# Kernel tuning notes

Measured on AMD Instinct MI355X. Metric: run time of the kernel, lower is better.

Reference implementation:

```python
import jax, jax.numpy as jnp
import numpy as np

N, E = 50000, 800000
F_IN, F_EMB1, F_EMB2, F_HID, F_OUT = 128, 512, 128, 1024, 64


def _linear_params(k, fan_in, fan_out):
    s = 1.0 / np.sqrt(fan_in)
    kw, kb = jax.random.split(k)
    W = jax.random.uniform(kw, (fan_in, fan_out), jnp.float32, -s, s)
    b = jax.random.uniform(kb, (fan_out,), jnp.float32, -s, s)
    return W, b


def setup_inputs() -> dict:
    key = jax.random.key(0)
    ks = jax.random.split(key, 8)
    x = jax.random.normal(ks[0], (N, F_IN), jnp.float32)
    src = jax.random.randint(ks[1], (E,), 0, N)
    dst = jax.random.randint(ks[2], (E,), 0, N)
    edge_index = jnp.stack([src, dst])  # [2, E]
    edge_weight = jax.random.uniform(ks[3], (E,), jnp.float32)  # positive weights
    W1, b1 = _linear_params(ks[4], F_IN, F_EMB1)
    W2, b2 = _linear_params(ks[5], F_EMB1, F_EMB2)
    W3, b3 = _linear_params(ks[6], F_EMB2, F_HID)
    W4, b4 = _linear_params(ks[7], F_HID, F_OUT)
    return dict(x=x, edge_index=edge_index, edge_weight=edge_weight,
                W1=W1, b1=b1, W2=W2, b2=b2, W3=W3, b3=b3, W4=W4, b4=b4)


def gcn_conv(x, src, dst, w, W, b):
    """PyG GCNConv: transform, then sym-normalized weighted aggregation with self-loops.
    out = D^{-1/2} (A_w + I) D^{-1/2} (x W) + b,  deg = scatter(w @ dst) + 1."""
    n = x.shape[0]
    h = x @ W  # [N, F_out]
    deg = jax.ops.segment_sum(w, dst, num_segments=n) + 1.0  # +1 for self-loop weight
    dinv = jax.lax.rsqrt(deg)
    norm = dinv[src] * w * dinv[dst]  # [E]
    agg = jax.ops.segment_sum(norm[:, None] * h[src], dst, num_segments=n)
    agg = agg + h / deg[:, None]  # self-loop: dinv[i]*1*dinv[i] * h[i]
    return agg + b


def reference(x, edge_index, edge_weight, W1, b1, W2, b2, W3, b3, W4, b4):
    src, dst = edge_index[0], edge_index[1]
    h = jax.nn.relu(gcn_conv(x, src, dst, edge_weight, W1, b1))
    # graph_normalization=False -> identity; dropout is identity in eval mode
    h = jax.nn.relu(gcn_conv(h, src, dst, edge_weight, W2, b2))
    h = jax.nn.relu(h @ W3 + b3)
    out = jax.nn.relu(h @ W4 + b4)
    return out
```

## Files before the change

kernel.cpp:

```cpp
#include <hip/hip_runtime.h>


#define ELLW 64

typedef short bf16x8 __attribute__((ext_vector_type(8)));
typedef float f32x4 __attribute__((ext_vector_type(4)));

__device__ __forceinline__ unsigned short f2b(float f) {
    unsigned u = __builtin_bit_cast(unsigned, f);
    unsigned r = (u + 0x7FFFu + ((u >> 16) & 1u)) >> 16;
    return (unsigned short)r;
}
__device__ __forceinline__ float b2f(unsigned short u) {
    return __builtin_bit_cast(float, (unsigned)u << 16);
}

__global__ void k_setup(const float* __restrict__ x,
                        const float* __restrict__ W1, const float* __restrict__ W2,
                        const float* __restrict__ W3, const float* __restrict__ W4,
                        unsigned short* __restrict__ W1t, unsigned short* __restrict__ W2t,
                        unsigned short* __restrict__ W3t, unsigned short* __restrict__ W4t,
                        unsigned short* __restrict__ xb,
                        const int* __restrict__ src, const int* __restrict__ dst,
                        const float* __restrict__ ew,
                        unsigned long long* __restrict__ cnt64,
                        int2* __restrict__ s_edge, int Nn, int E) {
    int b = blockIdx.x;
    if (b < 3125) {
        int e = b * 256 + threadIdx.x;
        if (e < E) {
            int d = dst[e];
            float wv = ew[e];
            unsigned wfix = (unsigned)(wv * 8388608.0f);
            unsigned long long add = ((unsigned long long)1 << 32) | wfix;
            unsigned long long old = atomicAdd(&cnt64[d], add);
            int slot = (int)(old >> 32);
            if (slot < ELLW)
                s_edge[(size_t)d * ELLW + slot] =
                    make_int2(src[e], __builtin_bit_cast(int, wv));
        }
    } else if (b < 4405) {
        int i = (b - 3125) * 256 + threadIdx.x;
        if (i < 65536) {
            int k = i >> 9, n = i & 511;
            W1t[n * 128 + k] = f2b(W1[i]);
        } else if (i < 131072) {
            int j = i - 65536; int k = j >> 7, n = j & 127;
            W2t[n * 512 + k] = f2b(W2[j]);
        } else if (i < 262144) {
            int j = i - 131072; int k = j >> 10, n = j & 1023;
            W3t[n * 128 + k] = f2b(W3[j]);
        } else {
            int j = i - 262144; int k = j >> 6, n = j & 63;
            W4t[n * 1024 + k] = f2b(W4[j]);
        }
    } else {
        int i = (b - 4405) * 256 + threadIdx.x;
        if (i < Nn * 32) {
            float4 v = ((const float4*)x)[i];
            ushort4 o;
            o.x = f2b(v.x); o.y = f2b(v.y); o.z = f2b(v.z); o.w = f2b(v.w);
            ((ushort4*)xb)[i] = o;
        }
    }
}

__global__ __launch_bounds__(256) void k_degscale(
    const unsigned long long* __restrict__ cnt64, float* __restrict__ dinv,
    unsigned short* __restrict__ xb, int Nn) {
    int node = blockIdx.x * 4 + (threadIdx.x >> 6);
    if (node >= Nn) return;
    int lane = threadIdx.x & 63;
    unsigned long long cv = cnt64[node];
    float deg = 1.0f + (float)(unsigned)(cv & 0xFFFFFFFFull) * (1.0f / 8388608.0f);
    float di = rsqrtf(deg);
    if (lane == 0) dinv[node] = di;
    ushort2 v = ((ushort2*)(xb + (size_t)node * 128))[lane];
    ushort2 o;
    o.x = f2b(b2f(v.x) * di);
    o.y = f2b(b2f(v.y) * di);
    ((ushort2*)(xb + (size_t)node * 128))[lane] = o;
}

template <bool BIAS_RELU>
__global__ __launch_bounds__(256) void k_gather(
    const unsigned short* __restrict__ Xb, const int2* __restrict__ s_edge,
    const unsigned long long* __restrict__ cnt64, const float* __restrict__ dinv,
    const float* __restrict__ bias, unsigned short* __restrict__ outb, int Nn) {
    int node = blockIdx.x * 4 + (threadIdx.x >> 6);
    if (node >= Nn) return;
    int lane = threadIdx.x & 63;
    float di = dinv[node];
    ushort2 sv = ((const ushort2*)(Xb + (size_t)node * 128))[lane];
    float ax = b2f(sv.x), ay = b2f(sv.y);

    int c = min((int)(cnt64[node] >> 32), ELLW);
    size_t base = (size_t)node * ELLW;
    int sreg = 0;
    float nv = 0.0f;
    if (lane < c) {
        int2 rec = s_edge[base + lane];
        sreg = rec.x;
        nv = __builtin_bit_cast(float, rec.y);
    }

    int j = 0;
    for (; j + 8 <= c; j += 8) {
        int s0 = __shfl(sreg, j),     s1 = __shfl(sreg, j + 1);
        int s2 = __shfl(sreg, j + 2), s3 = __shfl(sreg, j + 3);
        int s4 = __shfl(sreg, j + 4), s5 = __shfl(sreg, j + 5);
        int s6 = __shfl(sreg, j + 6), s7 = __shfl(sreg, j + 7);
        float n0 = __shfl(nv, j),     n1 = __shfl(nv, j + 1);
        float n2 = __shfl(nv, j + 2), n3 = __shfl(nv, j + 3);
        float n4 = __shfl(nv, j + 4), n5 = __shfl(nv, j + 5);
        float n6 = __shfl(nv, j + 6), n7 = __shfl(nv, j + 7);
        ushort2 r0 = ((const ushort2*)(Xb + (size_t)s0 * 128))[lane];
        ushort2 r1 = ((const ushort2*)(Xb + (size_t)s1 * 128))[lane];
        ushort2 r2 = ((const ushort2*)(Xb + (size_t)s2 * 128))[lane];
        ushort2 r3 = ((const ushort2*)(Xb + (size_t)s3 * 128))[lane];
        ushort2 r4 = ((const ushort2*)(Xb + (size_t)s4 * 128))[lane];
        ushort2 r5 = ((const ushort2*)(Xb + (size_t)s5 * 128))[lane];
        ushort2 r6 = ((const ushort2*)(Xb + (size_t)s6 * 128))[lane];
        ushort2 r7 = ((const ushort2*)(Xb + (size_t)s7 * 128))[lane];
        ax += n0 * b2f(r0.x) + n1 * b2f(r1.x) + n2 * b2f(r2.x) + n3 * b2f(r3.x);
        ay += n0 * b2f(r0.y) + n1 * b2f(r1.y) + n2 * b2f(r2.y) + n3 * b2f(r3.y);
        ax += n4 * b2f(r4.x) + n5 * b2f(r5.x) + n6 * b2f(r6.x) + n7 * b2f(r7.x);
        ay += n4 * b2f(r4.y) + n5 * b2f(r5.y) + n6 * b2f(r6.y) + n7 * b2f(r7.y);
    }
    for (; j < c; ++j) {
        int sj = __shfl(sreg, j);
        float nj = __shfl(nv, j);
        ushort2 r = ((const ushort2*)(Xb + (size_t)sj * 128))[lane];
        ax += nj * b2f(r.x);
        ay += nj * b2f(r.y);
    }

    ax *= di; ay *= di;
    if (BIAS_RELU) {
        float2 bv = ((const float2*)bias)[lane];
        ax = fmaxf(ax + bv.x, 0.0f);
        ay = fmaxf(ay + bv.y, 0.0f);
    }
    ushort2 o; o.x = f2b(ax); o.y = f2b(ay);
    ((ushort2*)(outb + (size_t)node * 128))[lane] = o;
}

template <int H, int OUTW, bool HAS_BO, bool OUT_BF16, bool SCALE_OUT>
__global__ __launch_bounds__(256) void k_mlp(
    const unsigned short* __restrict__ A, const unsigned short* __restrict__ Wht,
    const unsigned short* __restrict__ Wot, const float* __restrict__ bh,
    const float* __restrict__ bo, const float* __restrict__ dinv,
    void* __restrict__ out, int M) {
    constexpr int HC = H / 64;
    constexpr int NJ = OUTW / 16;
    constexpr int OW4 = OUTW / 32;
    __shared__ __align__(16) unsigned short Whs[64 * 128];
    __shared__ __align__(16) unsigned short Ps[128 * 64];
    __shared__ __align__(16) unsigned short Wos[OUTW * 64];
    const int tid = threadIdx.x, wave = tid >> 6, lane = tid & 63;
    const int lm = lane & 15, quad = lane >> 4;
    const int bm0 = blockIdx.x * 128;

    bf16x8 af[2][4];
    #pragma unroll
    for (int i = 0; i < 2; ++i) {
        int gr = bm0 + wave * 32 + i * 16 + lm;
        #pragma unroll
        for (int kb = 0; kb < 4; ++kb) af[i][kb] = bf16x8{0, 0, 0, 0, 0, 0, 0, 0};
        if (gr < M) {
            #pragma unroll
            for (int kb = 0; kb < 4; ++kb)
                af[i][kb] = *(const bf16x8*)(A + (size_t)gr * 128 + kb * 32 + quad * 8);
        }
    }

    #pragma unroll
    for (int u = 0; u < 4; ++u) {
        int idx = tid + u * 256; int r = idx >> 4, g = idx & 15;
        *(int4*)&Whs[r * 128 + ((g ^ (r & 15)) * 8)] =
            *(const int4*)(Wht + (size_t)r * 128 + g * 8);
    }
    #pragma unroll
    for (int u = 0; u < OW4; ++u) {
        int idx = tid + u * 256; int r = idx >> 3, g = idx & 7;
        *(int4*)&Wos[r * 64 + ((g ^ (r & 7)) * 8)] =
            *(const int4*)(Wot + (size_t)r * H + g * 8);
    }
    __syncthreads();

    f32x4 oacc[2][NJ] = {};
    for (int c = 0; c < HC; ++c) {
        f32x4 hacc[2][4] = {};
        #pragma unroll
        for (int kb = 0; kb < 4; ++kb) {
            bf16x8 bfr[4];
            #pragma unroll
            for (int j = 0; j < 4; ++j) {
                int r = j * 16 + lm, g = kb * 4 + quad;
                bfr[j] = *(const bf16x8*)&Whs[r * 128 + ((g ^ (r & 15)) * 8)];
            }
            #pragma unroll
            for (int i = 0; i < 2; ++i)
                #pragma unroll
                for (int j = 0; j < 4; ++j)
                    hacc[i][j] = __builtin_amdgcn_mfma_f32_16x16x32_bf16(
                        af[i][kb], bfr[j], hacc[i][j], 0, 0, 0);
        }

        #pragma unroll
        for (int i = 0; i < 2; ++i) {
            #pragma unroll
            for (int j = 0; j < 4; ++j) {
                int col = j * 16 + lm;
                float bv = bh[c * 64 + col];
                #pragma unroll
                for (int r4 = 0; r4 < 4; ++r4) {
                    int row = wave * 32 + i * 16 + quad * 4 + r4;
                    float o = fmaxf(hacc[i][j][r4] + bv, 0.0f);
                    Ps[row * 64 + (((col >> 3) ^ (row & 7)) * 8) + (col & 7)] = f2b(o);
                }
            }
        }

        #pragma unroll
        for (int kb = 0; kb < 2; ++kb) {
            bf16x8 pf[2];
            #pragma unroll
            for (int i = 0; i < 2; ++i) {
                int r = wave * 32 + i * 16 + lm, g = kb * 4 + quad;
                pf[i] = *(const bf16x8*)&Ps[r * 64 + ((g ^ (r & 7)) * 8)];
            }
            #pragma unroll
            for (int j = 0; j < NJ; ++j) {
                int r = j * 16 + lm, g = kb * 4 + quad;
                bf16x8 wf = *(const bf16x8*)&Wos[r * 64 + ((g ^ (r & 7)) * 8)];
                #pragma unroll
                for (int i = 0; i < 2; ++i)
                    oacc[i][j] = __builtin_amdgcn_mfma_f32_16x16x32_bf16(
                        pf[i], wf, oacc[i][j], 0, 0, 0);
            }
        }

        if (c + 1 < HC) {
            __syncthreads();
            #pragma unroll
            for (int u = 0; u < 4; ++u) {
                int idx = tid + u * 256; int r = idx >> 4, g = idx & 15;
                *(int4*)&Whs[r * 128 + ((g ^ (r & 15)) * 8)] =
                    *(const int4*)(Wht + (size_t)((c + 1) * 64 + r) * 128 + g * 8);
            }
            #pragma unroll
            for (int u = 0; u < OW4; ++u) {
                int idx = tid + u * 256; int r = idx >> 3, g = idx & 7;
                *(int4*)&Wos[r * 64 + ((g ^ (r & 7)) * 8)] =
                    *(const int4*)(Wot + (size_t)r * H + (c + 1) * 64 + g * 8);
            }
            __syncthreads();
        }
    }

    #pragma unroll
    for (int i = 0; i < 2; ++i) {
        #pragma unroll
        for (int j = 0; j < NJ; ++j) {
            int col = j * 16 + lm;
            float bv = HAS_BO ? bo[col] : 0.0f;
            #pragma unroll
            for (int r4 = 0; r4 < 4; ++r4) {
                int m = bm0 + wave * 32 + i * 16 + quad * 4 + r4;
                if (m < M) {
                    float o = oacc[i][j][r4];
                    if (SCALE_OUT) o *= dinv[m];
                    if (HAS_BO) o = fmaxf(o + bv, 0.0f);
                    if (OUT_BF16)
                        ((unsigned short*)out)[(size_t)m * OUTW + col] = f2b(o);
                    else
                        ((float*)out)[(size_t)m * OUTW + col] = o;
                }
            }
        }
    }
}

static inline int cdiv(long a, long b) { return (int)((a + b - 1) / b); }

extern "C" void kernel_launch(void* const* d_in, const int* in_sizes, int n_in,
                              void* d_out, int out_size, void* d_ws, size_t ws_size,
                              hipStream_t stream) {
    const float* x  = (const float*)d_in[0];
    const int*   ei = (const int*)d_in[1];
    const float* ew = (const float*)d_in[2];
    const float* W1 = (const float*)d_in[3];
    const float* b1 = (const float*)d_in[4];
    const float* W2 = (const float*)d_in[5];
    const float* b2 = (const float*)d_in[6];
    const float* W3 = (const float*)d_in[7];
    const float* b3 = (const float*)d_in[8];
    const float* W4 = (const float*)d_in[9];
    const float* b4 = (const float*)d_in[10];
    const int Nn = in_sizes[0] / 128;
    const int E  = in_sizes[1] / 2;
    const int* src = ei;
    const int* dst = ei + E;

    char* ws = (char*)d_ws;
    size_t off_b = 0;
    auto alloc = [&](size_t bytes) -> void* {
        void* p = ws + off_b;
        off_b += (bytes + 255) & ~(size_t)255;
        return p;
    };
    float*              dinv   = (float*)alloc((size_t)Nn * 4);
    unsigned long long* cnt64  = (unsigned long long*)alloc((size_t)Nn * 8);
    int2*               s_edge = (int2*)alloc((size_t)Nn * ELLW * 8);
    unsigned short*     W1t    = (unsigned short*)alloc(512 * 128 * 2);
    unsigned short*     W2t    = (unsigned short*)alloc(128 * 512 * 2);
    unsigned short*     W3t    = (unsigned short*)alloc(1024 * 128 * 2);
    unsigned short*     W4t    = (unsigned short*)alloc(64 * 1024 * 2);
    unsigned short*     xb     = (unsigned short*)alloc((size_t)Nn * 128 * 2);
    unsigned short*     t2b    = (unsigned short*)alloc((size_t)Nn * 128 * 2);
    unsigned short*     actb   = (unsigned short*)alloc((size_t)Nn * 128 * 2);
    float*              out    = (float*)d_out;

    hipMemsetAsync(cnt64, 0, (size_t)Nn * 8, stream);
    k_setup<<<10655, 256, 0, stream>>>(x, W1, W2, W3, W4, W1t, W2t, W3t, W4t,
                                       xb, src, dst, ew, cnt64, s_edge, Nn, E);
    k_degscale<<<cdiv(Nn, 4), 256, 0, stream>>>(cnt64, dinv, xb, Nn);

    k_gather<false><<<cdiv(Nn, 4), 256, 0, stream>>>(
        xb, s_edge, cnt64, dinv, nullptr, actb, Nn);
    k_mlp<512, 128, false, true, true><<<cdiv(Nn, 128), 256, 0, stream>>>(
        actb, W1t, W2t, b1, nullptr, dinv, t2b, Nn);

    k_gather<true><<<cdiv(Nn, 4), 256, 0, stream>>>(
        t2b, s_edge, cnt64, dinv, b2, actb, Nn);

    k_mlp<1024, 64, true, false, false><<<cdiv(Nn, 128), 256, 0, stream>>>(
        actb, W3t, W4t, b3, b4, nullptr, out, Nn);
}
```

Baseline: 318.7 us.

## Precompute per-edge symmetric norms in first gather and pad degree counters

The D^-1/2 scaling moves off node features and into per-edge weights. The first gather computes dinv[src]*w*dinv[dst] and writes it back into the ELL edge list, and the second gather reuses it. This drops the separate xb rescale pass and the dinv scaling in the MLP epilogue, at the cost of an extra random dinv read and a store per edge in the first gather. Degree counters are also padded to a 128-byte stride to cut atomic contention within a cache line, which makes the memset and k_deg reads 16x larger and strided.

```diff
diff --git a/kernel.cpp b/kernel.cpp
--- a/kernel.cpp
+++ b/kernel.cpp
@@ -2,6 +2,7 @@
 
 
 #define ELLW 64
+#define C64S 16
 
 typedef short bf16x8 __attribute__((ext_vector_type(8)));
 typedef float f32x4 __attribute__((ext_vector_type(4)));
@@ -33,7 +34,7 @@
             float wv = ew[e];
             unsigned wfix = (unsigned)(wv * 8388608.0f);
             unsigned long long add = ((unsigned long long)1 << 32) | wfix;
-            unsigned long long old = atomicAdd(&cnt64[d], add);
+            unsigned long long old = atomicAdd(&cnt64[(size_t)d * C64S], add);
             int slot = (int)(old >> 32);
             if (slot < ELLW)
                 s_edge[(size_t)d * ELLW + slot] =
@@ -65,43 +66,42 @@
     }
 }
 
-__global__ __launch_bounds__(256) void k_degscale(
-    const unsigned long long* __restrict__ cnt64, float* __restrict__ dinv,
-    unsigned short* __restrict__ xb, int Nn) {
-    int node = blockIdx.x * 4 + (threadIdx.x >> 6);
-    if (node >= Nn) return;
-    int lane = threadIdx.x & 63;
-    unsigned long long cv = cnt64[node];
+__global__ void k_deg(const unsigned long long* __restrict__ cnt64,
+                      float* __restrict__ dinv, int Nn) {
+    int i = blockIdx.x * 256 + threadIdx.x;
+    if (i >= Nn) return;
+    unsigned long long cv = cnt64[(size_t)i * C64S];
     float deg = 1.0f + (float)(unsigned)(cv & 0xFFFFFFFFull) * (1.0f / 8388608.0f);
-    float di = rsqrtf(deg);
-    if (lane == 0) dinv[node] = di;
-    ushort2 v = ((ushort2*)(xb + (size_t)node * 128))[lane];
-    ushort2 o;
-    o.x = f2b(b2f(v.x) * di);
-    o.y = f2b(b2f(v.y) * di);
-    ((ushort2*)(xb + (size_t)node * 128))[lane] = o;
-}
-
-template <bool BIAS_RELU>
+    dinv[i] = rsqrtf(deg);
+}
+
+template <bool FIRST, bool BIAS_RELU>
 __global__ __launch_bounds__(256) void k_gather(
-    const unsigned short* __restrict__ Xb, const int2* __restrict__ s_edge,
+    const unsigned short* __restrict__ Xb, int2* __restrict__ s_edge,
     const unsigned long long* __restrict__ cnt64, const float* __restrict__ dinv,
     const float* __restrict__ bias, unsigned short* __restrict__ outb, int Nn) {
     int node = blockIdx.x * 4 + (threadIdx.x >> 6);
     if (node >= Nn) return;
     int lane = threadIdx.x & 63;
     float di = dinv[node];
+    float dii = di * di;
     ushort2 sv = ((const ushort2*)(Xb + (size_t)node * 128))[lane];
-    float ax = b2f(sv.x), ay = b2f(sv.y);
-
-    int c = min((int)(cnt64[node] >> 32), ELLW);
+    float ax = b2f(sv.x) * dii, ay = b2f(sv.y) * dii;
+
+    int c = min((int)(cnt64[(size_t)node * C64S] >> 32), ELLW);
     size_t base = (size_t)node * ELLW;
     int sreg = 0;
     float nv = 0.0f;
     if (lane < c) {
         int2 rec = s_edge[base + lane];
         sreg = rec.x;
-        nv = __builtin_bit_cast(float, rec.y);
+        if (FIRST) {
+            float wv = __builtin_bit_cast(float, rec.y);
+            nv = dinv[sreg] * wv * di;
+            ((int*)s_edge)[2 * (base + lane) + 1] = __builtin_bit_cast(int, nv);
+        } else {
+            nv = __builtin_bit_cast(float, rec.y);
+        }
     }
 
     int j = 0;
@@ -135,7 +135,6 @@
         ay += nj * b2f(r.y);
     }
 
-    ax *= di; ay *= di;
     if (BIAS_RELU) {
         float2 bv = ((const float2*)bias)[lane];
         ax = fmaxf(ax + bv.x, 0.0f);
@@ -145,12 +144,11 @@
     ((ushort2*)(outb + (size_t)node * 128))[lane] = o;
 }
 
-template <int H, int OUTW, bool HAS_BO, bool OUT_BF16, bool SCALE_OUT>
+template <int H, int OUTW, bool HAS_BO, bool OUT_BF16>
 __global__ __launch_bounds__(256) void k_mlp(
     const unsigned short* __restrict__ A, const unsigned short* __restrict__ Wht,
     const unsigned short* __restrict__ Wot, const float* __restrict__ bh,
-    const float* __restrict__ bo, const float* __restrict__ dinv,
-    void* __restrict__ out, int M) {
+    const float* __restrict__ bo, void* __restrict__ out, int M) {
     constexpr int HC = H / 64;
     constexpr int NJ = OUTW / 16;
     constexpr int OW4 = OUTW / 32;
@@ -270,7 +268,6 @@
                 int m = bm0 + wave * 32 + i * 16 + quad * 4 + r4;
                 if (m < M) {
                     float o = oacc[i][j][r4];
-                    if (SCALE_OUT) o *= dinv[m];
                     if (HAS_BO) o = fmaxf(o + bv, 0.0f);
                     if (OUT_BF16)
                         ((unsigned short*)out)[(size_t)m * OUTW + col] = f2b(o);
@@ -311,7 +308,7 @@
         return p;
     };
     float*              dinv   = (float*)alloc((size_t)Nn * 4);
-    unsigned long long* cnt64  = (unsigned long long*)alloc((size_t)Nn * 8);
+    unsigned long long* cnt64  = (unsigned long long*)alloc((size_t)Nn * C64S * 8);
     int2*               s_edge = (int2*)alloc((size_t)Nn * ELLW * 8);
     unsigned short*     W1t    = (unsigned short*)alloc(512 * 128 * 2);
     unsigned short*     W2t    = (unsigned short*)alloc(128 * 512 * 2);
@@ -322,19 +319,19 @@
     unsigned short*     actb   = (unsigned short*)alloc((size_t)Nn * 128 * 2);
     float*              out    = (float*)d_out;
 
-    hipMemsetAsync(cnt64, 0, (size_t)Nn * 8, stream);
+    hipMemsetAsync(cnt64, 0, (size_t)Nn * C64S * 8, stream);
     k_setup<<<10655, 256, 0, stream>>>(x, W1, W2, W3, W4, W1t, W2t, W3t, W4t,
                                        xb, src, dst, ew, cnt64, s_edge, Nn, E);
-    k_degscale<<<cdiv(Nn, 4), 256, 0, stream>>>(cnt64, dinv, xb, Nn);
-
-    k_gather<false><<<cdiv(Nn, 4), 256, 0, stream>>>(
+    k_deg<<<cdiv(Nn, 256), 256, 0, stream>>>(cnt64, dinv, Nn);
+
+    k_gather<true, false><<<cdiv(Nn, 4), 256, 0, stream>>>(
         xb, s_edge, cnt64, dinv, nullptr, actb, Nn);
-    k_mlp<512, 128, false, true, true><<<cdiv(Nn, 128), 256, 0, stream>>>(
-        actb, W1t, W2t, b1, nullptr, dinv, t2b, Nn);
-
-    k_gather<true><<<cdiv(Nn, 4), 256, 0, stream>>>(
+    k_mlp<512, 128, false, true><<<cdiv(Nn, 128), 256, 0, stream>>>(
+        actb, W1t, W2t, b1, nullptr, t2b, Nn);
+
+    k_gather<false, true><<<cdiv(Nn, 4), 256, 0, stream>>>(
         t2b, s_edge, cnt64, dinv, b2, actb, Nn);
 
-    k_mlp<1024, 64, true, false, false><<<cdiv(Nn, 128), 256, 0, stream>>>(
-        actb, W3t, W4t, b3, b4, nullptr, out, Nn);
-}
+    k_mlp<1024, 64, true, false><<<cdiv(Nn, 128), 256, 0, stream>>>(
+        actb, W3t, W4t, b3, b4, out, Nn);
+}
```

After: 287.2 us. 1.11x faster.
